# Kernel tuning notes

Measured on AMD Instinct MI355X. Metric: run time of the kernel, lower is better.

The kernel has to match this reference:

```python
import jax, jax.numpy as jnp
import numpy as np

TEMPERATURE = 1.0
D_THRESH = 0.1
EPS = 1e-10
NORM_EPS = 1e-12  # F.normalize clamp


def _l2_normalize(x):
    n = jnp.sqrt(jnp.sum(x * x, axis=1, keepdims=True))
    return x / jnp.maximum(n, NORM_EPS)


def setup_inputs() -> dict:
    key = jax.random.key(0)
    k1, k2, k3 = jax.random.split(key, 3)
    N, D = 8192, 128
    f1 = jax.random.normal(k1, (N, D), dtype=jnp.float32)
    f2 = jax.random.normal(k2, (N, D), dtype=jnp.float32)
    # continuous targets in [-1, 1) so both the distance mask (|ti-tj|>0.1)
    # and the polarity mask (sign mismatch) are exercised
    targets = jax.random.uniform(k3, (N,), dtype=jnp.float32, minval=-1.0, maxval=1.0)
    return {"f1": f1, "f2": f2, "targets": targets}


def reference(f1, f2, targets):
    f1 = _l2_normalize(f1)
    f2 = _l2_normalize(f2)

    # self_mask: 1 where pair is a negative (far target or opposite polarity)
    dist_t = jnp.abs(targets[:, None] - targets[None, :])  # [N,N]
    mask_distance = dist_t > D_THRESH
    polarity = targets > 0
    mask_polarity = polarity[:, None] != polarity[None, :]
    self_mask = (mask_distance | mask_polarity).astype(f1.dtype)  # [N,N]

    # ||f1_i - f2_j||^2 via the cdist/matmul trick (avoids [N,N,D] tensor)
    sq1 = jnp.sum(f1 * f1, axis=1)  # [N]
    sq2 = jnp.sum(f2 * f2, axis=1)  # [N]
    dist = sq1[:, None] - 2.0 * (f1 @ f2.T) + sq2[None, :]  # [N,N]
    cos = 1.0 - 0.5 * dist

    p = jax.nn.softmax(cos / TEMPERATURE, axis=1)  # [N,N]
    pos_w = 1.0 - self_mask
    log_pos = -jnp.log(p + EPS) * pos_w
    log_neg = -jnp.log(1.0 - p + EPS) * self_mask
    per_row = (jnp.sum(log_pos, axis=1) / jnp.sum(pos_w, axis=1)
               + jnp.sum(log_neg, axis=1) / jnp.sum(self_mask, axis=1))
    return jnp.mean(per_row)
```

## Files before the change

kernel.cpp:

```cpp
#include <hip/hip_runtime.h>
#include <hip/hip_bf16.h>
#include <math.h>

#define NROWS 8192
#define DDIM  128
#define JCHUNKS 16
#define JPER  (NROWS / JCHUNKS)
#define STAGE_COLS 64
#define NSTAGES (JPER / STAGE_COLS)
#define ROWS_PER_BLOCK 256
#define GRIDX (NROWS / ROWS_PER_BLOCK)
#define LOG2E 1.44269504088896f

#define AS1 __attribute__((address_space(1)))
#define AS3 __attribute__((address_space(3)))

typedef __attribute__((ext_vector_type(8))) short bf16x8;
typedef __attribute__((ext_vector_type(4))) float f32x4;

__global__ __launch_bounds__(256) void norm_kernel(
    const float* __restrict__ f1, const float* __restrict__ f2,
    __hip_bfloat16* __restrict__ f1b, __hip_bfloat16* __restrict__ f2b,
    float* __restrict__ out) {
  if (blockIdx.x == 0 && threadIdx.x == 0) out[0] = 0.0f;
  int t = threadIdx.x;
  int rloc = t >> 5;
  int l = t & 31;
  int b = blockIdx.x;
  int half = (b >= NROWS / 8) ? 1 : 0;
  int row = (b - half * (NROWS / 8)) * 8 + rloc;
  const float* src = half ? f2 : f1;
  __hip_bfloat16* dst = half ? f2b : f1b;

  float4 v = ((const float4*)src)[row * (DDIM / 4) + l];
  float s = v.x * v.x + v.y * v.y + v.z * v.z + v.w * v.w;
  #pragma unroll
  for (int off = 1; off < 32; off <<= 1) s += __shfl_xor(s, off, 64);
  float inv = 1.0f / fmaxf(sqrtf(s), 1e-12f);
  __hip_bfloat16 hv[4];
  hv[0] = __float2bfloat16(v.x * inv);
  hv[1] = __float2bfloat16(v.y * inv);
  hv[2] = __float2bfloat16(v.z * inv);
  hv[3] = __float2bfloat16(v.w * inv);
  *(ushort4*)&dst[(size_t)row * DDIM + l * 4] = *(ushort4*)hv;
}

__global__ __launch_bounds__(512, 4) void stats_kernel(
    const __hip_bfloat16* __restrict__ f1b,
    const __hip_bfloat16* __restrict__ f2b,
    const float* __restrict__ targets,
    float* __restrict__ partials) {
  __shared__ __align__(16) char lds0[STAGE_COLS * 256];
  __shared__ __align__(16) char lds1[STAGE_COLS * 256];
  __shared__ __align__(16) float tsh[JPER];

  const int chunk = blockIdx.y;
  const int i0 = blockIdx.x * ROWS_PER_BLOCK;
  const int w    = threadIdx.x >> 6;
  const int lane = threadIdx.x & 63;
  const int p15  = lane & 15;
  const int rl4  = lane >> 4;
  const int rbase = i0 + w * 32;

  bf16x8 afrag[2][4];
  #pragma unroll
  for (int rs = 0; rs < 2; ++rs) {
    const __hip_bfloat16* arow =
        &f1b[(size_t)(rbase + rs * 16 + p15) * DDIM + rl4 * 8];
    #pragma unroll
    for (int ks = 0; ks < 4; ++ks)
      afrag[rs][ks] = *(const bf16x8*)(arow + ks * 32);
  }

  f32x4 ki[2];
  #pragma unroll
  for (int rs = 0; rs < 2; ++rs)
    #pragma unroll
    for (int rr = 0; rr < 4; ++rr)
      ki[rs][rr] = targets[rbase + rs * 16 + rl4 * 4 + rr];

  f32x4 Z[2], Zp[2], Cp[2], Np[2];
  #pragma unroll
  for (int rs = 0; rs < 2; ++rs) {
    Z[rs] = (f32x4){0.f, 0.f, 0.f, 0.f};
    Zp[rs] = (f32x4){0.f, 0.f, 0.f, 0.f};
    Cp[rs] = (f32x4){0.f, 0.f, 0.f, 0.f};
    Np[rs] = (f32x4){0.f, 0.f, 0.f, 0.f};
  }

  const int jb0 = chunk * JPER;

  int srcoff[2];
  #pragma unroll
  for (int q = 0; q < 2; ++q) {
    int rloc = w * 8 + q * 4 + rl4;
    int c    = p15 ^ (rloc & 15);
    srcoff[q] = rloc * DDIM + c * 8;
  }

  {
    __builtin_amdgcn_global_load_lds(
        (const AS1 void*)(targets + jb0 + w * 64 + lane),
        (AS3 void*)(&tsh[w * 64]), 4, 0, 0);
    const __hip_bfloat16* gstage = f2b + (size_t)jb0 * DDIM;
    char* lbase = &lds0[w * 2048];
    #pragma unroll
    for (int q = 0; q < 2; ++q)
      __builtin_amdgcn_global_load_lds((const AS1 void*)(gstage + srcoff[q]),
                                       (AS3 void*)(lbase + q * 1024), 16, 0, 0);
  }

  for (int s = 0; s < NSTAGES; ++s) {
    __syncthreads();

    if (s + 1 < NSTAGES) {
      const __hip_bfloat16* gstage = f2b + (size_t)(jb0 + (s + 1) * STAGE_COLS) * DDIM;
      char* lbase = ((s + 1) & 1) ? &lds1[w * 2048] : &lds0[w * 2048];
      #pragma unroll
      for (int q = 0; q < 2; ++q)
        __builtin_amdgcn_global_load_lds((const AS1 void*)(gstage + srcoff[q]),
                                         (AS3 void*)(lbase + q * 1024), 16, 0, 0);
    }

    const char* lb = (s & 1) ? lds1 : lds0;
    #pragma unroll
    for (int ct = 0; ct < 4; ++ct) {
      const int rloc = ct * 16 + p15;
      bf16x8 bfrag[4];
      #pragma unroll
      for (int ks = 0; ks < 4; ++ks)
        bfrag[ks] = *(const bf16x8*)(lb + rloc * 256 + (((rl4 + ks * 4) ^ p15) << 4));

      float tj = tsh[s * STAGE_COLS + ct * 16 + p15];
      const bool pj = tj > 0.0f;
      const f32x4 tj4 = {tj, tj, tj, tj};
      const f32x4 K4  = {LOG2E, LOG2E, LOG2E, LOG2E};

      #pragma unroll
      for (int rs = 0; rs < 2; ++rs) {
        f32x4 acc = {0.f, 0.f, 0.f, 0.f};
        #pragma unroll
        for (int ks = 0; ks < 4; ++ks)
          acc = __builtin_amdgcn_mfma_f32_16x16x32_bf16(afrag[rs][ks], bfrag[ks], acc, 0, 0, 0);

        f32x4 c4 = acc;
        f32x4 d4 = ki[rs] - tj4;
        f32x4 m4;
        #pragma unroll
        for (int rr = 0; rr < 4; ++rr) {
          bool q = (__builtin_fabsf(d4[rr]) <= 0.1f) & ((ki[rs][rr] > 0.0f) == pj);
          m4[rr] = q ? 1.0f : 0.0f;
        }
        f32x4 x4 = c4 * K4 - K4;
        f32x4 e4;
        #pragma unroll
        for (int rr = 0; rr < 4; ++rr) e4[rr] = __builtin_amdgcn_exp2f(x4[rr]);
        Z[rs]  += e4;
        Zp[rs] += m4 * e4;
        Cp[rs] += m4 * c4;
        Np[rs] += m4;
      }
    }
  }

  #pragma unroll
  for (int rs = 0; rs < 2; ++rs) {
    #pragma unroll
    for (int rr = 0; rr < 4; ++rr) {
      #pragma unroll
      for (int off = 1; off < 16; off <<= 1) {
        Z[rs][rr]  += __shfl_xor(Z[rs][rr],  off, 64);
        Zp[rs][rr] += __shfl_xor(Zp[rs][rr], off, 64);
        Cp[rs][rr] += __shfl_xor(Cp[rs][rr], off, 64);
        Np[rs][rr] += __shfl_xor(Np[rs][rr], off, 64);
      }
    }
  }
  if (p15 == 0) {
    #pragma unroll
    for (int rs = 0; rs < 2; ++rs)
      #pragma unroll
      for (int rr = 0; rr < 4; ++rr) {
        size_t row = rbase + rs * 16 + rl4 * 4 + rr;
        f32x4 st = {Z[rs][rr], Zp[rs][rr], Cp[rs][rr], Np[rs][rr]};
        *(f32x4*)&partials[((size_t)row * JCHUNKS + chunk) * 4] = st;
      }
  }
}

__global__ void finalize_rows(const float* __restrict__ partials,
                              float* __restrict__ out) {
  int r = blockIdx.x * 256 + threadIdx.x;
  float Z = 0, Zp = 0, Cp = 0, Np = 0;
  for (int ch = 0; ch < JCHUNKS; ++ch) {
    float4 p = *(const float4*)&partials[((size_t)r * JCHUNKS + ch) * 4];
    Z += p.x; Zp += p.y; Cp += p.z; Np += p.w;
  }
  float Zn = Z - Zp;
  float nn = (float)NROWS - Np;
  float spos = (1.0f + logf(Z)) - Cp / Np;
  float sneg = Zn / Z - nn * 1e-10f;
  float per_row = spos + sneg / nn;

  float v = per_row;
  for (int off = 32; off; off >>= 1) v += __shfl_xor(v, off, 64);
  __shared__ float wsum[4];
  int lane = threadIdx.x & 63, wid = threadIdx.x >> 6;
  if (lane == 0) wsum[wid] = v;
  __syncthreads();
  if (threadIdx.x == 0)
    atomicAdd(out, (wsum[0] + wsum[1] + wsum[2] + wsum[3]) * (1.0f / (float)NROWS));
}

extern "C" void kernel_launch(void* const* d_in, const int* in_sizes, int n_in,
                              void* d_out, int out_size, void* d_ws, size_t ws_size,
                              hipStream_t stream) {
  const float* f1  = (const float*)d_in[0];
  const float* f2  = (const float*)d_in[1];
  const float* tgt = (const float*)d_in[2];
  float* out = (float*)d_out;

  char* ws = (char*)d_ws;
  __hip_bfloat16* f1b = (__hip_bfloat16*)ws;
  __hip_bfloat16* f2b = (__hip_bfloat16*)(ws + (size_t)NROWS * DDIM * 2);
  float* partials = (float*)(ws + (size_t)NROWS * DDIM * 4);

  norm_kernel<<<2 * (NROWS / 8), 256, 0, stream>>>(f1, f2, f1b, f2b, out);
  dim3 g2(GRIDX, JCHUNKS);
  stats_kernel<<<g2, 512, 0, stream>>>(f1b, f2b, tgt, partials);
  finalize_rows<<<NROWS / 256, 256, 0, stream>>>(partials, out);
}
```

Measured before the change: 98.22 us.

## Double stage width to 128 columns and use packed float2 epilogue math

```diff
diff --git a/kernel.cpp b/kernel.cpp
--- a/kernel.cpp
+++ b/kernel.cpp
@@ -6,7 +6,7 @@
 #define DDIM  128
 #define JCHUNKS 16
 #define JPER  (NROWS / JCHUNKS)
-#define STAGE_COLS 64
+#define STAGE_COLS 128
 #define NSTAGES (JPER / STAGE_COLS)
 #define ROWS_PER_BLOCK 256
 #define GRIDX (NROWS / ROWS_PER_BLOCK)
@@ -17,6 +17,7 @@
 
 typedef __attribute__((ext_vector_type(8))) short bf16x8;
 typedef __attribute__((ext_vector_type(4))) float f32x4;
+typedef __attribute__((ext_vector_type(2))) float f32x2;
 
 __global__ __launch_bounds__(256) void norm_kernel(
     const float* __restrict__ f1, const float* __restrict__ f2,
@@ -45,7 +46,7 @@
   *(ushort4*)&dst[(size_t)row * DDIM + l * 4] = *(ushort4*)hv;
 }
 
-__global__ __launch_bounds__(512, 4) void stats_kernel(
+__global__ __launch_bounds__(512, 3) void stats_kernel(
     const __hip_bfloat16* __restrict__ f1b,
     const __hip_bfloat16* __restrict__ f2b,
     const float* __restrict__ targets,
@@ -72,28 +73,32 @@
       afrag[rs][ks] = *(const bf16x8*)(arow + ks * 32);
   }
 
-  f32x4 ki[2];
+  f32x2 ki2[2][2];
   #pragma unroll
   for (int rs = 0; rs < 2; ++rs)
     #pragma unroll
-    for (int rr = 0; rr < 4; ++rr)
-      ki[rs][rr] = targets[rbase + rs * 16 + rl4 * 4 + rr];
-
-  f32x4 Z[2], Zp[2], Cp[2], Np[2];
-  #pragma unroll
-  for (int rs = 0; rs < 2; ++rs) {
-    Z[rs] = (f32x4){0.f, 0.f, 0.f, 0.f};
-    Zp[rs] = (f32x4){0.f, 0.f, 0.f, 0.f};
-    Cp[rs] = (f32x4){0.f, 0.f, 0.f, 0.f};
-    Np[rs] = (f32x4){0.f, 0.f, 0.f, 0.f};
-  }
+    for (int h = 0; h < 2; ++h) {
+      ki2[rs][h][0] = targets[rbase + rs * 16 + rl4 * 4 + 2 * h + 0];
+      ki2[rs][h][1] = targets[rbase + rs * 16 + rl4 * 4 + 2 * h + 1];
+    }
+
+  f32x2 Z2[2][2], Zp2[2][2], Cp2[2][2], Np2[2][2];
+  #pragma unroll
+  for (int rs = 0; rs < 2; ++rs)
+    #pragma unroll
+    for (int h = 0; h < 2; ++h) {
+      Z2[rs][h] = (f32x2){0.f, 0.f};
+      Zp2[rs][h] = (f32x2){0.f, 0.f};
+      Cp2[rs][h] = (f32x2){0.f, 0.f};
+      Np2[rs][h] = (f32x2){0.f, 0.f};
+    }
 
   const int jb0 = chunk * JPER;
 
-  int srcoff[2];
-  #pragma unroll
-  for (int q = 0; q < 2; ++q) {
-    int rloc = w * 8 + q * 4 + rl4;
+  int srcoff[4];
+  #pragma unroll
+  for (int q = 0; q < 4; ++q) {
+    int rloc = w * 16 + q * 4 + rl4;
     int c    = p15 ^ (rloc & 15);
     srcoff[q] = rloc * DDIM + c * 8;
   }
@@ -103,9 +108,9 @@
         (const AS1 void*)(targets + jb0 + w * 64 + lane),
         (AS3 void*)(&tsh[w * 64]), 4, 0, 0);
     const __hip_bfloat16* gstage = f2b + (size_t)jb0 * DDIM;
-    char* lbase = &lds0[w * 2048];
-    #pragma unroll
-    for (int q = 0; q < 2; ++q)
+    char* lbase = &lds0[w * 4096];
+    #pragma unroll
+    for (int q = 0; q < 4; ++q)
       __builtin_amdgcn_global_load_lds((const AS1 void*)(gstage + srcoff[q]),
                                        (AS3 void*)(lbase + q * 1024), 16, 0, 0);
   }
@@ -115,16 +120,16 @@
 
     if (s + 1 < NSTAGES) {
       const __hip_bfloat16* gstage = f2b + (size_t)(jb0 + (s + 1) * STAGE_COLS) * DDIM;
-      char* lbase = ((s + 1) & 1) ? &lds1[w * 2048] : &lds0[w * 2048];
-      #pragma unroll
-      for (int q = 0; q < 2; ++q)
+      char* lbase = ((s + 1) & 1) ? &lds1[w * 4096] : &lds0[w * 4096];
+      #pragma unroll
+      for (int q = 0; q < 4; ++q)
         __builtin_amdgcn_global_load_lds((const AS1 void*)(gstage + srcoff[q]),
                                          (AS3 void*)(lbase + q * 1024), 16, 0, 0);
     }
 
     const char* lb = (s & 1) ? lds1 : lds0;
     #pragma unroll
-    for (int ct = 0; ct < 4; ++ct) {
+    for (int ct = 0; ct < 8; ++ct) {
       const int rloc = ct * 16 + p15;
       bf16x8 bfrag[4];
       #pragma unroll
@@ -133,8 +138,8 @@
 
       float tj = tsh[s * STAGE_COLS + ct * 16 + p15];
       const bool pj = tj > 0.0f;
-      const f32x4 tj4 = {tj, tj, tj, tj};
-      const f32x4 K4  = {LOG2E, LOG2E, LOG2E, LOG2E};
+      const f32x2 tj2 = {tj, tj};
+      const f32x2 K2  = {LOG2E, LOG2E};
 
       #pragma unroll
       for (int rs = 0; rs < 2; ++rs) {
@@ -143,48 +148,48 @@
         for (int ks = 0; ks < 4; ++ks)
           acc = __builtin_amdgcn_mfma_f32_16x16x32_bf16(afrag[rs][ks], bfrag[ks], acc, 0, 0, 0);
 
-        f32x4 c4 = acc;
-        f32x4 d4 = ki[rs] - tj4;
-        f32x4 m4;
-        #pragma unroll
-        for (int rr = 0; rr < 4; ++rr) {
-          bool q = (__builtin_fabsf(d4[rr]) <= 0.1f) & ((ki[rs][rr] > 0.0f) == pj);
-          m4[rr] = q ? 1.0f : 0.0f;
+        #pragma unroll
+        for (int h = 0; h < 2; ++h) {
+          f32x2 c2 = {acc[2 * h + 0], acc[2 * h + 1]};
+          f32x2 d2 = ki2[rs][h] - tj2;
+          bool q0 = (__builtin_fabsf(d2[0]) <= 0.1f) & ((ki2[rs][h][0] > 0.0f) == pj);
+          bool q1 = (__builtin_fabsf(d2[1]) <= 0.1f) & ((ki2[rs][h][1] > 0.0f) == pj);
+          f32x2 m2 = {q0 ? 1.0f : 0.0f, q1 ? 1.0f : 0.0f};
+          f32x2 x2 = c2 * K2 - K2;
+          f32x2 e2 = {__builtin_amdgcn_exp2f(x2[0]), __builtin_amdgcn_exp2f(x2[1])};
+          Z2[rs][h]  += e2;
+          Zp2[rs][h] += m2 * e2;
+          Cp2[rs][h] += m2 * c2;
+          Np2[rs][h] += m2;
         }
-        f32x4 x4 = c4 * K4 - K4;
-        f32x4 e4;
-        #pragma unroll
-        for (int rr = 0; rr < 4; ++rr) e4[rr] = __builtin_amdgcn_exp2f(x4[rr]);
-        Z[rs]  += e4;
-        Zp[rs] += m4 * e4;
-        Cp[rs] += m4 * c4;
-        Np[rs] += m4;
       }
     }
   }
 
   #pragma unroll
-  for (int rs = 0; rs < 2; ++rs) {
-    #pragma unroll
-    for (int rr = 0; rr < 4; ++rr) {
-      #pragma unroll
-      for (int off = 1; off < 16; off <<= 1) {
-        Z[rs][rr]  += __shfl_xor(Z[rs][rr],  off, 64);
-        Zp[rs][rr] += __shfl_xor(Zp[rs][rr], off, 64);
-        Cp[rs][rr] += __shfl_xor(Cp[rs][rr], off, 64);
-        Np[rs][rr] += __shfl_xor(Np[rs][rr], off, 64);
-      }
-    }
-  }
+  for (int rs = 0; rs < 2; ++rs)
+    #pragma unroll
+    for (int h = 0; h < 2; ++h)
+      #pragma unroll
+      for (int c = 0; c < 2; ++c)
+        #pragma unroll
+        for (int off = 1; off < 16; off <<= 1) {
+          Z2[rs][h][c]  += __shfl_xor(Z2[rs][h][c],  off, 64);
+          Zp2[rs][h][c] += __shfl_xor(Zp2[rs][h][c], off, 64);
+          Cp2[rs][h][c] += __shfl_xor(Cp2[rs][h][c], off, 64);
+          Np2[rs][h][c] += __shfl_xor(Np2[rs][h][c], off, 64);
+        }
   if (p15 == 0) {
     #pragma unroll
     for (int rs = 0; rs < 2; ++rs)
       #pragma unroll
-      for (int rr = 0; rr < 4; ++rr) {
-        size_t row = rbase + rs * 16 + rl4 * 4 + rr;
-        f32x4 st = {Z[rs][rr], Zp[rs][rr], Cp[rs][rr], Np[rs][rr]};
-        *(f32x4*)&partials[((size_t)row * JCHUNKS + chunk) * 4] = st;
-      }
+      for (int h = 0; h < 2; ++h)
+        #pragma unroll
+        for (int c = 0; c < 2; ++c) {
+          size_t row = rbase + rs * 16 + rl4 * 4 + 2 * h + c;
+          f32x4 st = {Z2[rs][h][c], Zp2[rs][h][c], Cp2[rs][h][c], Np2[rs][h][c]};
+          *(f32x4*)&partials[((size_t)row * JCHUNKS + chunk) * 4] = st;
+        }
   }
 }
 
```

Result: slower. 105.1 us (+7.0%).
